# Kernel tuning notes

Hardware: AMD Instinct MI355X
Metric: run time of the kernel (lower is better)

## Reference

```python
import jax, jax.numpy as jnp
import numpy as np

N, C, B, NPG, M, E = 131072, 128, 64, 2048, 64, 1048576
LN_EPS = 1e-5


def setup_inputs() -> dict:
    key = jax.random.key(0)
    ks = jax.random.split(key, 8)
    h = jax.random.normal(ks[0], (N, C), dtype=jnp.float32)
    edge_index = jax.random.randint(ks[1], (2, E), 0, N, dtype=jnp.int32)
    U = jax.random.normal(ks[2], (B, NPG, M), dtype=jnp.float32)
    W = jax.random.normal(ks[3], (M, C, C), dtype=jnp.float32) * 0.02
    lin_w = jax.random.normal(ks[4], (C, C), dtype=jnp.float32) * (1.0 / np.sqrt(C))
    lin_b = jax.random.normal(ks[5], (C,), dtype=jnp.float32) * 0.01
    ln_g = jnp.ones((C,), dtype=jnp.float32)
    ln_beta = jnp.zeros((C,), dtype=jnp.float32)
    return {"h": h, "U": U, "W": W, "lin_w": lin_w, "lin_b": lin_b,
            "ln_g": ln_g, "ln_beta": ln_beta, "edge_index": edge_index}


def _gfno_block(h, U, W, lin_w, lin_b, ln_g, ln_beta, edge_index):
    n_nodes, c = h.shape
    b, npg, m_avail = U.shape
    m = min(m_avail, W.shape[0])
    Um = U[:, :, :m]                      # [B, n, m]
    Wm = W[:m]                            # [m, C, C]
    # Block-diagonal spectral conv (equal-sized graphs -> batched einsum)
    hb = h.reshape(b, npg, c)             # [B, n, C]
    h_hat = jnp.einsum('bnm,bnc->bmc', Um, hb)        # U^T h per graph
    out_hat = jnp.einsum('bmc,mco->bmo', h_hat, Wm)   # per-mode mixing
    spec = jnp.einsum('bnm,bmo->bno', Um, out_hat).reshape(n_nodes, c)
    # Local scatter-mean aggregation
    src, dst = edge_index[0], edge_index[1]
    agg = jax.ops.segment_sum(h[src], dst, num_segments=n_nodes)   # [N, C]
    deg = jax.ops.segment_sum(jnp.ones((src.shape[0],), h.dtype), dst,
                              num_segments=n_nodes)
    deg = jnp.maximum(deg, 1.0)[:, None]
    local = (agg / deg) @ lin_w.T + lin_b
    # Residual + LayerNorm + GELU (exact, erf-based as torch default)
    x = h + spec + local
    mu = jnp.mean(x, axis=-1, keepdims=True)
    var = jnp.mean(jnp.square(x - mu), axis=-1, keepdims=True)
    xn = (x - mu) * jax.lax.rsqrt(var + LN_EPS) * ln_g + ln_beta
    return jax.nn.gelu(xn, approximate=False)


def reference(h, U, W, lin_w, lin_b, ln_g, ln_beta, edge_index):
    return _gfno_block(h, U, W, lin_w, lin_b, ln_g, ln_beta, edge_index)
```

## Files before the change

### kernel.cpp

```cpp
#include <hip/hip_runtime.h>
#include <math.h>

#define NN   131072
#define CN   128
#define BN   64
#define NPGN 2048
#define MN   64
#define EN   1048576

typedef unsigned short u16;
typedef unsigned int   u32;
typedef __attribute__((ext_vector_type(8))) short short8;
typedef __attribute__((ext_vector_type(4))) float f32x4;

__device__ __forceinline__ float bf2f(u16 u){ return __uint_as_float(((u32)u)<<16); }
__device__ __forceinline__ u16 f2bf(float f){
  u32 x = __float_as_uint(f);
  return (u16)((x + 0x7fffu + ((x>>16)&1u)) >> 16);
}

__global__ void k_count(const int* __restrict__ dst, int* __restrict__ deg){
  int e = blockIdx.x*256 + threadIdx.x;
  atomicAdd(&deg[dst[e]], 1);
}

__global__ void k_scan1(const int* __restrict__ deg, int* __restrict__ rowst, int* __restrict__ bsum){
  __shared__ int s[512];
  const int t = threadIdx.x;
  const int i = blockIdx.x*512 + t;
  int v = deg[i];
  s[t] = v;
  __syncthreads();
  for (int off=1; off<512; off<<=1){
    int a = (t>=off) ? s[t-off] : 0;
    __syncthreads();
    s[t] += a;
    __syncthreads();
  }
  rowst[i] = s[t] - v;
  if (t==511) bsum[blockIdx.x] = s[511];
}

__global__ void k_scan2(const int* __restrict__ bsum, int* __restrict__ bofs){
  __shared__ int s[256];
  const int t = threadIdx.x;
  int v = bsum[t];
  s[t] = v;
  __syncthreads();
  for (int off=1; off<256; off<<=1){
    int a = (t>=off) ? s[t-off] : 0;
    __syncthreads();
    s[t] += a;
    __syncthreads();
  }
  bofs[t] = s[t] - v;
}

__global__ void k_scan3(int* __restrict__ rowst, const int* __restrict__ bofs){
  int i = blockIdx.x*256 + threadIdx.x;
  rowst[i] += bofs[i>>9];
}

__global__ void k_fill(const int* __restrict__ src, const int* __restrict__ dst,
                       const int* __restrict__ rowst, int* __restrict__ cursor,
                       int* __restrict__ csr){
  int e = blockIdx.x*256 + threadIdx.x;
  int d = dst[e];
  int p = atomicAdd(&cursor[d], 1);
  csr[rowst[d] + p] = src[e];
}

__global__ void k_prepw(const float* __restrict__ lin_w, u16* __restrict__ wsw){
  int tid = blockIdx.x*256 + threadIdx.x;
  int g = tid >> 6, L = tid & 63;
  int ct = g >> 2, ks = g & 3;
  int o = L & 15, q = L >> 4;
  const float* srcp = lin_w + (ct*16+o)*CN + ks*32 + q*8;
  u16 tmp[8];
  #pragma unroll
  for (int j=0;j<8;++j) tmp[j] = f2bf(srcp[j]);
  *(uint4*)(wsw + (size_t)tid*8) = *(const uint4*)tmp;
}

__global__ void k_prepWT(const float* __restrict__ W, u16* __restrict__ WT16){
  __shared__ u16 st[128*132];
  const int t = threadIdx.x;
  const int m = blockIdx.x;
  const float* Wm = W + (size_t)m*CN*CN;
  #pragma unroll
  for (int it=0; it<16; ++it){
    int flat = (it*256 + t)*4;
    int c = flat >> 7, o = flat & 127;
    float4 v = *(const float4*)(Wm + flat);
    st[(o+0)*132 + c] = f2bf(v.x);
    st[(o+1)*132 + c] = f2bf(v.y);
    st[(o+2)*132 + c] = f2bf(v.z);
    st[(o+3)*132 + c] = f2bf(v.w);
  }
  __syncthreads();
  u16* dstm = WT16 + (size_t)m*CN*CN;
  #pragma unroll
  for (int it=0; it<8; ++it){
    int oidx = (it*256 + t)*8;
    int o = oidx >> 7, c = oidx & 127;
    uint4 v = *(const uint4*)&st[o*132 + c];
    *(uint4*)(dstm + (size_t)o*CN + c) = v;
  }
}

__global__ void k_prep_h(const float* __restrict__ h, u16* __restrict__ h16, u16* __restrict__ ht16){
  __shared__ u16 st[CN*72];
  const int t = threadIdx.x;
  const int b = blockIdx.x >> 5;
  const int n0 = (blockIdx.x & 31)*64;
  const float* srcb = h + ((size_t)b*NPGN + n0)*CN;
  u16* natb = h16 + ((size_t)b*NPGN + n0)*CN;
  #pragma unroll
  for (int j=0;j<8;++j){
    int fidx = (j*256+t)*4;
    int r = fidx>>7, c = fidx&127;
    float4 v = *(const float4*)(srcb + fidx);
    u16 q0=f2bf(v.x), q1=f2bf(v.y), q2=f2bf(v.z), q3=f2bf(v.w);
    ushort4 nv; nv.x=q0; nv.y=q1; nv.z=q2; nv.w=q3;
    *(ushort4*)(natb + fidx) = nv;
    st[(c+0)*72 + r] = q0; st[(c+1)*72 + r] = q1;
    st[(c+2)*72 + r] = q2; st[(c+3)*72 + r] = q3;
  }
  __syncthreads();
  #pragma unroll
  for (int j=0;j<4;++j){
    int oidx = (j*256+t)*8;
    int c = oidx>>6, nn = oidx&63;
    uint4 v = *(const uint4*)&st[c*72 + nn];
    *(uint4*)(ht16 + ((size_t)b*CN + c)*NPGN + n0 + nn) = v;
  }
}

__global__ void k_prep_U(const float* __restrict__ U, u16* __restrict__ U16, u16* __restrict__ Ut16){
  __shared__ u16 st2[MN*136];
  const int t = threadIdx.x;
  const int b = blockIdx.x >> 4;
  const int n0 = (blockIdx.x & 15)*128;
  const float* srcb = U + ((size_t)b*NPGN + n0)*MN;
  u16* natb = U16 + ((size_t)b*NPGN + n0)*MN;
  #pragma unroll
  for (int j=0;j<8;++j){
    int fidx = (j*256+t)*4;
    int r = fidx>>6, mm = fidx&63;
    float4 v = *(const float4*)(srcb + fidx);
    u16 q0=f2bf(v.x), q1=f2bf(v.y), q2=f2bf(v.z), q3=f2bf(v.w);
    ushort4 nv; nv.x=q0; nv.y=q1; nv.z=q2; nv.w=q3;
    *(ushort4*)(natb + fidx) = nv;
    st2[(mm+0)*136 + r] = q0; st2[(mm+1)*136 + r] = q1;
    st2[(mm+2)*136 + r] = q2; st2[(mm+3)*136 + r] = q3;
  }
  __syncthreads();
  #pragma unroll
  for (int j=0;j<4;++j){
    int oidx = (j*256+t)*8;
    int mm = oidx>>7, nn = oidx&127;
    uint4 v = *(const uint4*)&st2[mm*136 + nn];
    *(uint4*)(Ut16 + ((size_t)b*MN + mm)*NPGN + n0 + nn) = v;
  }
}

__global__ __launch_bounds__(256) void k_hhat(const u16* __restrict__ Ut16,
                                              const u16* __restrict__ ht16,
                                              float* __restrict__ hp){
  const int t = threadIdx.x;
  const int L = t & 63, w = t >> 6;
  const int b = blockIdx.x >> 3, q = blockIdx.x & 7;
  const int lo = L & 15, qd = (L >> 4) << 3;
  f32x4 acc[8] = {};
  const u16* Arow  = Ut16 + ((size_t)(b*MN + w*16 + lo))*NPGN + q*256 + qd;
  const u16* Bbase = ht16 + ((size_t)(b*CN + lo))*NPGN + q*256 + qd;
  #pragma unroll
  for (int ks=0; ks<8; ++ks){
    short8 af = *(const short8*)(Arow + ks*32);
    #pragma unroll
    for (int ct=0; ct<8; ++ct){
      short8 bf = *(const short8*)(Bbase + (size_t)ct*16*NPGN + ks*32);
      acc[ct] = __builtin_amdgcn_mfma_f32_16x16x32_bf16(af, bf, acc[ct], 0, 0, 0);
    }
  }
  const int rb = w*16 + ((L>>4)<<2);
  float* dstb = hp + ((size_t)q*BN + b)*MN*CN;
  #pragma unroll
  for (int ct=0; ct<8; ++ct)
    #pragma unroll
    for (int r=0; r<4; ++r)
      dstb[(size_t)(rb+r)*CN + ct*16 + lo] = acc[ct][r];
}

__global__ __launch_bounds__(256) void k_ohat(const float* __restrict__ hp,
                                              const u16* __restrict__ WT16,
                                              u16* __restrict__ ohatT){
  __shared__ u16 shHi[16*132];
  __shared__ u16 shLo[16*132];
  const int t = threadIdx.x;
  const int m  = blockIdx.x >> 2;
  const int bq = blockIdx.x & 3;

  {
    const int bl = t >> 4;
    const int c0 = (t & 15) * 8;
    const size_t S = (size_t)BN*MN*CN;
    const float* base = hp + ((size_t)(bq*16 + bl)*MN + m)*CN + c0;
    float a[8] = {0,0,0,0,0,0,0,0};
    #pragma unroll
    for (int q=0; q<8; ++q){
      float4 v0 = *(const float4*)(base + q*S);
      float4 v1 = *(const float4*)(base + q*S + 4);
      a[0]+=v0.x; a[1]+=v0.y; a[2]+=v0.z; a[3]+=v0.w;
      a[4]+=v1.x; a[5]+=v1.y; a[6]+=v1.z; a[7]+=v1.w;
    }
    u16 hi[8], lo[8];
    #pragma unroll
    for (int j=0;j<8;++j){
      hi[j] = f2bf(a[j]);
      lo[j] = f2bf(a[j] - bf2f(hi[j]));
    }
    *(uint4*)&shHi[bl*132 + c0] = *(const uint4*)hi;
    *(uint4*)&shLo[bl*132 + c0] = *(const uint4*)lo;
  }
  __syncthreads();

  const int L = t & 63, w = t >> 6;
  const int lo16 = L & 15, qd = (L >> 4) << 3;
  const u16* WTm = WT16 + (size_t)m*CN*CN;
  f32x4 acc[2] = {};
  #pragma unroll
  for (int ks=0; ks<4; ++ks){
    short8 ah = *(const short8*)&shHi[lo16*132 + ks*32 + qd];
    short8 al = *(const short8*)&shLo[lo16*132 + ks*32 + qd];
    #pragma unroll
    for (int ot=0; ot<2; ++ot){
      short8 bf = *(const short8*)(WTm + (size_t)(w*32 + ot*16 + lo16)*CN + ks*32 + qd);
      acc[ot] = __builtin_amdgcn_mfma_f32_16x16x32_bf16(ah, bf, acc[ot], 0, 0, 0);
      acc[ot] = __builtin_amdgcn_mfma_f32_16x16x32_bf16(al, bf, acc[ot], 0, 0, 0);
    }
  }
  const int rb = (L>>4)<<2;
  #pragma unroll
  for (int ot=0; ot<2; ++ot){
    #pragma unroll
    for (int r=0; r<4; ++r){
      int b = bq*16 + rb + r;
      int o = w*32 + ot*16 + lo16;
      ohatT[((size_t)b*CN + o)*MN + m] = f2bf(acc[ot][r]);
    }
  }
}

__device__ __forceinline__ void unp_add(float* a, uint4 p){
  a[0]+=bf2f((u16)(p.x&0xffffu)); a[1]+=bf2f((u16)(p.x>>16));
  a[2]+=bf2f((u16)(p.y&0xffffu)); a[3]+=bf2f((u16)(p.y>>16));
  a[4]+=bf2f((u16)(p.z&0xffffu)); a[5]+=bf2f((u16)(p.z>>16));
  a[6]+=bf2f((u16)(p.w&0xffffu)); a[7]+=bf2f((u16)(p.w>>16));
}

__global__ __launch_bounds__(256,6) void k_localep(
    const u16* __restrict__ h16, const u16* __restrict__ U16,
    const u16* __restrict__ ohatT, const u16* __restrict__ wsw,
    const int* __restrict__ rowst, const int* __restrict__ deg, const int* __restrict__ csr,
    const float* __restrict__ lin_b, const float* __restrict__ ln_g,
    const float* __restrict__ ln_beta, float* __restrict__ out){
  __shared__ u16 sv[32*136];
  __shared__ u16 sx16[32*132];
  const int t = threadIdx.x;
  const int w = t>>6, lane = t&63;
  const size_t n0 = (size_t)blockIdx.x*32;

  {
    const int g   = lane >> 4;
    const int c16 = lane & 15;
    #pragma unroll
    for (int p=0; p<4; ++p){
      const int iA = p*8 + w;
      const int iB = p*8 + 4 + w;
      const int nA = (int)n0 + iA, nB = (int)n0 + iB;
      const int rsA = rowst[nA], dgA = deg[nA];
      const int rsB = rowst[nB], dgB = deg[nB];
      const int reA = rsA + dgA, reB = rsB + dgB;
      int eA = rsA + g, eB = rsB + g;
      float accA[8] = {0.f,0.f,0.f,0.f,0.f,0.f,0.f,0.f};
      float accB[8] = {0.f,0.f,0.f,0.f,0.f,0.f,0.f,0.f};
      while (eA < reA || eB < reB){
        const bool vA0 = eA   < reA, vA1 = eA+4 < reA;
        const bool vB0 = eB   < reB, vB1 = eB+4 < reB;
        int sA0 = vA0 ? csr[eA]   : 0;
        int sA1 = vA1 ? csr[eA+4] : 0;
        int sB0 = vB0 ? csr[eB]   : 0;
        int sB1 = vB1 ? csr[eB+4] : 0;
        uint4 qA0 = {0u,0u,0u,0u}, qA1 = {0u,0u,0u,0u};
        uint4 qB0 = {0u,0u,0u,0u}, qB1 = {0u,0u,0u,0u};
        if (vA0) qA0 = *(const uint4*)(h16 + (size_t)sA0*CN + c16*8);
        if (vA1) qA1 = *(const uint4*)(h16 + (size_t)sA1*CN + c16*8);
        if (vB0) qB0 = *(const uint4*)(h16 + (size_t)sB0*CN + c16*8);
        if (vB1) qB1 = *(const uint4*)(h16 + (size_t)sB1*CN + c16*8);
        unp_add(accA, qA0); unp_add(accA, qA1);
        unp_add(accB, qB0); unp_add(accB, qB1);
        eA += 8; eB += 8;
      }
      #pragma unroll
      for (int j=0;j<8;++j){
        accA[j] += __shfl_xor(accA[j],16); accA[j] += __shfl_xor(accA[j],32);
        accB[j] += __shfl_xor(accB[j],16); accB[j] += __shfl_xor(accB[j],32);
      }
      const float invA = 1.0f / fmaxf((float)dgA, 1.0f);
      const float invB = 1.0f / fmaxf((float)dgB, 1.0f);
      if (g==0){
        u16 ta[8], tb[8];
        #pragma unroll
        for (int j=0;j<8;++j){ ta[j]=f2bf(accA[j]*invA); tb[j]=f2bf(accB[j]*invB); }
        *(uint4*)&sv[iA*136 + c16*8] = *(const uint4*)ta;
        *(uint4*)&sv[iB*136 + c16*8] = *(const uint4*)tb;
      }
    }
  }
  __syncthreads();

  const int rt = w&1, cb = w>>1;
  const int lo16 = lane & 15, qd = (lane>>4)<<3;
  f32x4 acc[4] = {};
  #pragma unroll
  for (int ks=0; ks<4; ++ks){
    short8 af = *(const short8*)&sv[(rt*16 + lo16)*136 + ks*32 + qd];
    #pragma unroll
    for (int c4=0; c4<4; ++c4){
      const short8 bf = *(const short8*)(wsw + ((size_t)((cb*4+c4)*4+ks)*64 + lane)*8);
      acc[c4] = __builtin_amdgcn_mfma_f32_16x16x32_bf16(af, bf, acc[c4], 0, 0, 0);
    }
  }
  {
    const int b = (int)(n0 >> 11);
    const u16* Au = U16  + ((size_t)(n0 + rt*16 + lo16))*MN + qd;
    const u16* Bu = ohatT + ((size_t)(b*CN + cb*64 + lo16))*MN + qd;
    #pragma unroll
    for (int ks=0; ks<2; ++ks){
      short8 af = *(const short8*)(Au + ks*32);
      #pragma unroll
      for (int c4=0; c4<4; ++c4){
        short8 bf = *(const short8*)(Bu + (size_t)c4*16*MN + ks*32);
        acc[c4] = __builtin_amdgcn_mfma_f32_16x16x32_bf16(af, bf, acc[c4], 0, 0, 0);
      }
    }
  }
  #pragma unroll
  for (int c4=0; c4<4; ++c4){
    int col = cb*64 + c4*16 + lo16;
    int rb = rt*16 + ((lane>>4)<<2);
    #pragma unroll
    for (int r=0; r<4; ++r) sx16[(rb+r)*132 + col] = f2bf(acc[c4][r]);
  }
  __syncthreads();

  float2 lb    = *(const float2*)(lin_b  + 2*lane);
  float2 lg    = *(const float2*)(ln_g   + 2*lane);
  float2 lbe   = *(const float2*)(ln_beta+ 2*lane);
  for (int r=0; r<8; ++r){
    int i = r*4 + w;
    size_t base = (n0 + i)*CN + 2*lane;
    u32 hA = *(const u32*)(h16 + base);
    u32 lA = *(const u32*)&sx16[i*132 + 2*lane];
    float x0 = bf2f((u16)(hA&0xffffu)) + bf2f((u16)(lA&0xffffu)) + lb.x;
    float x1 = bf2f((u16)(hA>>16))     + bf2f((u16)(lA>>16))     + lb.y;
    float s  = x0 + x1;
    float ss = fmaf(x0,x0, x1*x1);
    #pragma unroll
    for (int d=1; d<64; d<<=1){ s += __shfl_xor(s,d); ss += __shfl_xor(ss,d); }
    float mu  = s*(1.0f/128.0f);
    float var = ss*(1.0f/128.0f) - mu*mu;
    float rstd = rsqrtf(var + 1e-5f);
    float xn0 = (x0-mu)*rstd*lg.x + lbe.x;
    float xn1 = (x1-mu)*rstd*lg.y + lbe.y;
    float2 st;
    st.x = 0.5f*xn0*(1.0f + erff(xn0*0.70710678118654752f));
    st.y = 0.5f*xn1*(1.0f + erff(xn1*0.70710678118654752f));
    *(float2*)(out + base) = st;
  }
}

extern "C" void kernel_launch(void* const* d_in, const int* in_sizes, int n_in,
                              void* d_out, int out_size, void* d_ws, size_t ws_size,
                              hipStream_t stream) {
  const float* h      = (const float*)d_in[0];
  const float* U      = (const float*)d_in[1];
  const float* W      = (const float*)d_in[2];
  const float* lin_w  = (const float*)d_in[3];
  const float* lin_b  = (const float*)d_in[4];
  const float* ln_g   = (const float*)d_in[5];
  const float* ln_b2  = (const float*)d_in[6];
  const int* ei       = (const int*)d_in[7];
  const int* src = ei;
  const int* dst = ei + EN;
  float* out = (float*)d_out;

  char* wp = (char*)d_ws;
  float* hp     = (float*)wp; wp += (size_t)8*BN*MN*CN*sizeof(float);
  u16*   ohatT  = (u16*)wp;   wp += (size_t)BN*CN*MN*sizeof(u16);
  u16*   h16    = (u16*)wp;   wp += (size_t)NN*CN*sizeof(u16);
  u16*   ht16   = (u16*)wp;   wp += (size_t)BN*CN*NPGN*sizeof(u16);
  u16*   U16b   = (u16*)wp;   wp += (size_t)BN*NPGN*MN*sizeof(u16);
  u16*   Ut16   = (u16*)wp;   wp += (size_t)BN*MN*NPGN*sizeof(u16);
  u16*   wsw    = (u16*)wp;   wp += (size_t)CN*CN*sizeof(u16);
  u16*   WT16   = (u16*)wp;   wp += (size_t)MN*CN*CN*sizeof(u16);
  int*   deg    = (int*)wp;   wp += (size_t)NN*sizeof(int);
  int*   rowst  = (int*)wp;   wp += (size_t)NN*sizeof(int);
  int*   cursor = (int*)wp;   wp += (size_t)NN*sizeof(int);
  int*   csr    = (int*)wp;   wp += (size_t)EN*sizeof(int);
  int*   bsum   = (int*)wp;   wp += 512*sizeof(int);
  int*   bofs   = (int*)wp;   wp += 512*sizeof(int);

  hipMemsetAsync(deg,    0, (size_t)NN*sizeof(int), stream);
  hipMemsetAsync(cursor, 0, (size_t)NN*sizeof(int), stream);

  k_count<<<EN/256, 256, 0, stream>>>(dst, deg);
  k_scan1<<<NN/512, 512, 0, stream>>>(deg, rowst, bsum);
  k_scan2<<<1, 256, 0, stream>>>(bsum, bofs);
  k_scan3<<<NN/256, 256, 0, stream>>>(rowst, bofs);
  k_fill<<<EN/256, 256, 0, stream>>>(src, dst, rowst, cursor, csr);

  k_prepw<<<8, 256, 0, stream>>>(lin_w, wsw);
  k_prepWT<<<MN, 256, 0, stream>>>(W, WT16);
  k_prep_h<<<BN*32, 256, 0, stream>>>(h, h16, ht16);
  k_prep_U<<<BN*16, 256, 0, stream>>>(U, U16b, Ut16);

  k_hhat<<<BN*8, 256, 0, stream>>>(Ut16, ht16, hp);
  k_ohat<<<MN*4, 256, 0, stream>>>(hp, WT16, ohatT);

  k_localep<<<NN/32, 256, 0, stream>>>(h16, U16b, ohatT, wsw, rowst, deg, csr,
                                       lin_b, ln_g, ln_b2, out);
}
```

Baseline: 401.5 us.

## Split hhat channels across blocks and reorganize neighbor gather by channel slice

k_hhat now splits the 128 output channels into two halves across separate blocks, doubling the grid to 1024 blocks and halving accumulators per thread for better occupancy. In k_localep, the gather is restructured: each wave handles a 32-channel slice for all 32 nodes, with 8 lanes per edge row loading 8-byte chunks and up to 16 edges processed in a fixed unrolled step before a rarely-taken tail loop. This is meant to expose more memory-level parallelism for average degree ~8 and cut loop overhead, at the cost of smaller per-lane loads and more shuffle reductions. Launch bounds occupancy hint drops from 6 to 5.

```diff
diff --git a/kernel.cpp b/kernel.cpp
--- a/kernel.cpp
+++ b/kernel.cpp
@@ -169,16 +169,18 @@
                                               float* __restrict__ hp){
   const int t = threadIdx.x;
   const int L = t & 63, w = t >> 6;
-  const int b = blockIdx.x >> 3, q = blockIdx.x & 7;
+  const int b  = blockIdx.x >> 4;
+  const int q  = (blockIdx.x >> 1) & 7;
+  const int ch = blockIdx.x & 1;
   const int lo = L & 15, qd = (L >> 4) << 3;
-  f32x4 acc[8] = {};
+  f32x4 acc[4] = {};
   const u16* Arow  = Ut16 + ((size_t)(b*MN + w*16 + lo))*NPGN + q*256 + qd;
-  const u16* Bbase = ht16 + ((size_t)(b*CN + lo))*NPGN + q*256 + qd;
+  const u16* Bbase = ht16 + ((size_t)(b*CN + ch*64 + lo))*NPGN + q*256 + qd;
   #pragma unroll
   for (int ks=0; ks<8; ++ks){
     short8 af = *(const short8*)(Arow + ks*32);
     #pragma unroll
-    for (int ct=0; ct<8; ++ct){
+    for (int ct=0; ct<4; ++ct){
       short8 bf = *(const short8*)(Bbase + (size_t)ct*16*NPGN + ks*32);
       acc[ct] = __builtin_amdgcn_mfma_f32_16x16x32_bf16(af, bf, acc[ct], 0, 0, 0);
     }
@@ -186,10 +188,10 @@
   const int rb = w*16 + ((L>>4)<<2);
   float* dstb = hp + ((size_t)q*BN + b)*MN*CN;
   #pragma unroll
-  for (int ct=0; ct<8; ++ct)
+  for (int ct=0; ct<4; ++ct)
     #pragma unroll
     for (int r=0; r<4; ++r)
-      dstb[(size_t)(rb+r)*CN + ct*16 + lo] = acc[ct][r];
+      dstb[(size_t)(rb+r)*CN + ch*64 + ct*16 + lo] = acc[ct][r];
 }
 
 __global__ __launch_bounds__(256) void k_ohat(const float* __restrict__ hp,
@@ -252,14 +254,7 @@
   }
 }
 
-__device__ __forceinline__ void unp_add(float* a, uint4 p){
-  a[0]+=bf2f((u16)(p.x&0xffffu)); a[1]+=bf2f((u16)(p.x>>16));
-  a[2]+=bf2f((u16)(p.y&0xffffu)); a[3]+=bf2f((u16)(p.y>>16));
-  a[4]+=bf2f((u16)(p.z&0xffffu)); a[5]+=bf2f((u16)(p.z>>16));
-  a[6]+=bf2f((u16)(p.w&0xffffu)); a[7]+=bf2f((u16)(p.w>>16));
-}
-
-__global__ __launch_bounds__(256,6) void k_localep(
+__global__ __launch_bounds__(256,5) void k_localep(
     const u16* __restrict__ h16, const u16* __restrict__ U16,
     const u16* __restrict__ ohatT, const u16* __restrict__ wsw,
     const int* __restrict__ rowst, const int* __restrict__ deg, const int* __restrict__ csr,
@@ -272,49 +267,40 @@
   const size_t n0 = (size_t)blockIdx.x*32;
 
   {
-    const int g   = lane >> 4;
-    const int c16 = lane & 15;
-    #pragma unroll
-    for (int p=0; p<4; ++p){
-      const int iA = p*8 + w;
-      const int iB = p*8 + 4 + w;
-      const int nA = (int)n0 + iA, nB = (int)n0 + iB;
-      const int rsA = rowst[nA], dgA = deg[nA];
-      const int rsB = rowst[nB], dgB = deg[nB];
-      const int reA = rsA + dgA, reB = rsB + dgB;
-      int eA = rsA + g, eB = rsB + g;
-      float accA[8] = {0.f,0.f,0.f,0.f,0.f,0.f,0.f,0.f};
-      float accB[8] = {0.f,0.f,0.f,0.f,0.f,0.f,0.f,0.f};
-      while (eA < reA || eB < reB){
-        const bool vA0 = eA   < reA, vA1 = eA+4 < reA;
-        const bool vB0 = eB   < reB, vB1 = eB+4 < reB;
-        int sA0 = vA0 ? csr[eA]   : 0;
-        int sA1 = vA1 ? csr[eA+4] : 0;
-        int sB0 = vB0 ? csr[eB]   : 0;
-        int sB1 = vB1 ? csr[eB+4] : 0;
-        uint4 qA0 = {0u,0u,0u,0u}, qA1 = {0u,0u,0u,0u};
-        uint4 qB0 = {0u,0u,0u,0u}, qB1 = {0u,0u,0u,0u};
-        if (vA0) qA0 = *(const uint4*)(h16 + (size_t)sA0*CN + c16*8);
-        if (vA1) qA1 = *(const uint4*)(h16 + (size_t)sA1*CN + c16*8);
-        if (vB0) qB0 = *(const uint4*)(h16 + (size_t)sB0*CN + c16*8);
-        if (vB1) qB1 = *(const uint4*)(h16 + (size_t)sB1*CN + c16*8);
-        unp_add(accA, qA0); unp_add(accA, qA1);
-        unp_add(accB, qB0); unp_add(accB, qB1);
-        eA += 8; eB += 8;
+    const int g  = lane >> 3;
+    const int c8 = lane & 7;
+    const u16* hrow = h16 + w*32 + c8*4;
+    #pragma unroll 4
+    for (int i=0; i<32; ++i){
+      const int node = (int)n0 + i;
+      const int rs = rowst[node], dg = deg[node];
+      const bool v1 = g < dg, v2 = g+8 < dg;
+      int i1 = v1 ? csr[rs+g]   : 0;
+      int i2 = v2 ? csr[rs+8+g] : 0;
+      uint2 r1 = {0u,0u}, r2 = {0u,0u};
+      if (v1) r1 = *(const uint2*)(hrow + (size_t)i1*CN);
+      if (v2) r2 = *(const uint2*)(hrow + (size_t)i2*CN);
+      float a0 = bf2f((u16)(r1.x&0xffffu)) + bf2f((u16)(r2.x&0xffffu));
+      float a1 = bf2f((u16)(r1.x>>16))     + bf2f((u16)(r2.x>>16));
+      float a2 = bf2f((u16)(r1.y&0xffffu)) + bf2f((u16)(r2.y&0xffffu));
+      float a3 = bf2f((u16)(r1.y>>16))     + bf2f((u16)(r2.y>>16));
+      if (__builtin_expect(dg > 16, 0)){
+        for (int e = rs + 16 + g; e < rs + dg; e += 8){
+          int ii = csr[e];
+          uint2 r = *(const uint2*)(hrow + (size_t)ii*CN);
+          a0 += bf2f((u16)(r.x&0xffffu)); a1 += bf2f((u16)(r.x>>16));
+          a2 += bf2f((u16)(r.y&0xffffu)); a3 += bf2f((u16)(r.y>>16));
+        }
       }
-      #pragma unroll
-      for (int j=0;j<8;++j){
-        accA[j] += __shfl_xor(accA[j],16); accA[j] += __shfl_xor(accA[j],32);
-        accB[j] += __shfl_xor(accB[j],16); accB[j] += __shfl_xor(accB[j],32);
-      }
-      const float invA = 1.0f / fmaxf((float)dgA, 1.0f);
-      const float invB = 1.0f / fmaxf((float)dgB, 1.0f);
-      if (g==0){
-        u16 ta[8], tb[8];
-        #pragma unroll
-        for (int j=0;j<8;++j){ ta[j]=f2bf(accA[j]*invA); tb[j]=f2bf(accB[j]*invB); }
-        *(uint4*)&sv[iA*136 + c16*8] = *(const uint4*)ta;
-        *(uint4*)&sv[iB*136 + c16*8] = *(const uint4*)tb;
+      a0 += __shfl_xor(a0,8);  a1 += __shfl_xor(a1,8);  a2 += __shfl_xor(a2,8);  a3 += __shfl_xor(a3,8);
+      a0 += __shfl_xor(a0,16); a1 += __shfl_xor(a1,16); a2 += __shfl_xor(a2,16); a3 += __shfl_xor(a3,16);
+      a0 += __shfl_xor(a0,32); a1 += __shfl_xor(a1,32); a2 += __shfl_xor(a2,32); a3 += __shfl_xor(a3,32);
+      const float inv = 1.0f / fmaxf((float)dg, 1.0f);
+      if (g == 0){
+        u32 p0 = (u32)f2bf(a0*inv) | ((u32)f2bf(a1*inv) << 16);
+        u32 p1 = (u32)f2bf(a2*inv) | ((u32)f2bf(a3*inv) << 16);
+        uint2 pk; pk.x = p0; pk.y = p1;
+        *(uint2*)&sv[i*136 + w*32 + c8*4] = pk;
       }
     }
   }
@@ -426,7 +412,7 @@
   k_prep_h<<<BN*32, 256, 0, stream>>>(h, h16, ht16);
   k_prep_U<<<BN*16, 256, 0, stream>>>(U, U16b, Ut16);
 
-  k_hhat<<<BN*8, 256, 0, stream>>>(Ut16, ht16, hp);
+  k_hhat<<<BN*16, 256, 0, stream>>>(Ut16, ht16, hp);
   k_ohat<<<MN*4, 256, 0, stream>>>(hp, WT16, ohatT);
 
   k_localep<<<NN/32, 256, 0, stream>>>(h16, U16b, ohatT, wsw, rowst, deg, csr,
```

New measurement: 433.2 us. 1.08x slower.
